# Optimization experiments

Measured on AMD Instinct MI355X. Metric: run time of the kernel, lower is better.

The kernel has to match this reference:

```python
import jax, jax.numpy as jnp
import numpy as np

N_NODES = 100_000
N_EDGES = 1_200_000
IN_C, HID_C, OUT_C, K = 64, 64, 32, 3


def setup_inputs() -> dict:
    key = jax.random.key(0)
    ks = jax.random.split(key, 8)
    x = jax.random.normal(ks[0], (N_NODES, IN_C), dtype=jnp.float32)
    edge_index = jax.random.randint(ks[1], (2, N_EDGES), 0, N_NODES, dtype=jnp.int64)
    # ChebConv parameters: weight [K, in, out], bias [out] (Glorot-ish scale)
    W1 = jax.random.normal(ks[2], (K, IN_C, HID_C), dtype=jnp.float32) / np.sqrt(IN_C)
    b1 = jnp.zeros((HID_C,), dtype=jnp.float32)
    W2 = jax.random.normal(ks[3], (K, HID_C, OUT_C), dtype=jnp.float32) / np.sqrt(HID_C)
    b2 = jnp.zeros((OUT_C,), dtype=jnp.float32)
    return {"x": x, "edge_index": edge_index, "W1": W1, "b1": b1, "W2": W2, "b2": b2}


def _cheb_conv(x, row, col, norm_w, W, b):
    # Scaled Laplacian with lambda_max=2 (PyG default): L_hat = -D^{-1/2} A D^{-1/2}
    def prop(t):  # L_hat @ t, via edge gather + segment-sum scatter
        msg = norm_w[:, None] * t[col]            # [E, C]
        return -jax.ops.segment_sum(msg, row, num_segments=N_NODES)

    Tx0 = x
    out = Tx0 @ W[0]
    Tx1 = prop(x)
    out = out + Tx1 @ W[1]
    for k in range(2, W.shape[0]):
        Tx2 = 2.0 * prop(Tx1) - Tx0          # Chebyshev recurrence
        out = out + Tx2 @ W[k]
        Tx0, Tx1 = Tx1, Tx2
    return out + b


def reference(x, edge_index, W1, b1, W2, b2):
    row, col = edge_index[0], edge_index[1]
    deg = jax.ops.segment_sum(jnp.ones((row.shape[0],), x.dtype), row,
                              num_segments=N_NODES)
    deg_inv_sqrt = jnp.where(deg > 0, jax.lax.rsqrt(jnp.maximum(deg, 1.0)), 0.0)
    norm_w = deg_inv_sqrt[row] * deg_inv_sqrt[col]   # symmetric normalization

    h = jax.nn.relu(_cheb_conv(x, row, col, norm_w, W1, b1))
    # dropout omitted (eval mode / training=False)
    return _cheb_conv(h, row, col, norm_w, W2, b2)
```

## Files before the change

### kernel.cpp

```cpp
#include <hip/hip_runtime.h>
#include <hip/hip_fp16.h>

#define N_NODES_C 100000
#define N_EDGES_C 1200000
#define NBUK ((N_NODES_C + 255) >> 8)
#define CHUNK 4096

typedef _Float16 f16x8 __attribute__((ext_vector_type(8)));
typedef float f32x4 __attribute__((ext_vector_type(4)));

__global__ __launch_bounds__(256) void hist_f2h(const int* __restrict__ ei,
                                                int* __restrict__ bucket_cnt,
                                                const float* __restrict__ x,
                                                __half* __restrict__ xh,
                                                int nedges, int n4, int histB) {
    __shared__ int cnt[NBUK];
    const int tid = threadIdx.x;
    if (blockIdx.x < histB) {
        const int base = blockIdx.x * CHUNK;
        const int nloc = min(CHUNK, nedges - base);
        for (int i = tid; i < NBUK; i += 256) cnt[i] = 0;
        __syncthreads();
        for (int i = tid; i < nloc; i += 256) atomicAdd(&cnt[ei[base + i] >> 8], 1);
        __syncthreads();
        for (int b = tid; b < NBUK; b += 256) {
            int n = cnt[b];
            if (n) atomicAdd(&bucket_cnt[b], n);
        }
    } else {
        int i = (blockIdx.x - histB) * 256 + tid;
        if (i < n4) {
            float4 v = ((const float4*)x)[i];
            __half2 tmp[2];
            tmp[0] = __floats2half2_rn(v.x, v.y);
            tmp[1] = __floats2half2_rn(v.z, v.w);
            ((float2*)xh)[i] = *(float2*)tmp;
        }
    }
}

__global__ __launch_bounds__(256) void bucket_scan(const int* __restrict__ bucket_cnt,
                                                   int* __restrict__ bucket_base,
                                                   int* __restrict__ bucket_next, int nb) {
    __shared__ int s[256];
    const int tid = threadIdx.x;
    int a0 = (2 * tid < nb) ? bucket_cnt[2 * tid] : 0;
    int a1 = (2 * tid + 1 < nb) ? bucket_cnt[2 * tid + 1] : 0;
    s[tid] = a0 + a1;
    __syncthreads();
    for (int off = 1; off < 256; off <<= 1) {
        int v = s[tid];
        int add = (tid >= off) ? s[tid - off] : 0;
        __syncthreads();
        s[tid] = v + add;
        __syncthreads();
    }
    int excl = (tid > 0) ? s[tid - 1] : 0;
    if (2 * tid < nb) { bucket_base[2 * tid] = excl; bucket_next[2 * tid] = excl; }
    if (2 * tid + 1 < nb) { bucket_base[2 * tid + 1] = excl + a0; bucket_next[2 * tid + 1] = excl + a0; }
    if (tid == 255) bucket_base[nb] = s[255];
}

__global__ __launch_bounds__(256) void bin_stage(const int* __restrict__ ei,
                                                 int* __restrict__ bucket_next,
                                                 int2* __restrict__ staged, int nedges) {
    __shared__ int cnt[NBUK];
    __shared__ int ofs[NBUK];
    __shared__ int run[NBUK];
    __shared__ int gbase[NBUK];
    __shared__ int ssum[256];
    __shared__ int2 sedge[CHUNK];
    const int tid = threadIdx.x;
    const int base = blockIdx.x * CHUNK;
    const int nloc = min(CHUNK, nedges - base);

    for (int i = tid; i < NBUK; i += 256) { cnt[i] = 0; run[i] = 0; }
    __syncthreads();

    int r[16], c[16];
#pragma unroll
    for (int k = 0; k < 16; ++k) {
        int loc = tid + k * 256;
        bool ok = loc < nloc;
        int idx = base + loc;
        r[k] = ok ? ei[idx] : -1;
        c[k] = ok ? ei[nedges + idx] : 0;
        if (ok) atomicAdd(&cnt[r[k] >> 8], 1);
    }
    __syncthreads();

    int a0 = (2 * tid < NBUK) ? cnt[2 * tid] : 0;
    int a1 = (2 * tid + 1 < NBUK) ? cnt[2 * tid + 1] : 0;
    ssum[tid] = a0 + a1;
    __syncthreads();
    for (int off = 1; off < 256; off <<= 1) {
        int v = ssum[tid];
        int add = (tid >= off) ? ssum[tid - off] : 0;
        __syncthreads();
        ssum[tid] = v + add;
        __syncthreads();
    }
    int excl = (tid > 0) ? ssum[tid - 1] : 0;
    if (2 * tid < NBUK) ofs[2 * tid] = excl;
    if (2 * tid + 1 < NBUK) ofs[2 * tid + 1] = excl + a0;
    __syncthreads();

#pragma unroll
    for (int k = 0; k < 16; ++k) {
        if (r[k] >= 0) {
            int b = r[k] >> 8;
            int p = atomicAdd(&run[b], 1);
            sedge[ofs[b] + p] = make_int2(r[k], c[k]);
        }
    }
    __syncthreads();

    for (int b = tid; b < NBUK; b += 256) {
        int n = cnt[b];
        gbase[b] = n ? atomicAdd(&bucket_next[b], n) : 0;
    }
    __syncthreads();

    for (int i = tid; i < nloc; i += 256) {
        int2 e = sedge[i];
        int b = e.x >> 8;
        staged[gbase[b] + (i - ofs[b])] = e;
    }
}

__global__ __launch_bounds__(256) void bin_count(const int2* __restrict__ staged,
                                                 const int* __restrict__ bucket_base,
                                                 int* __restrict__ rowptr, float* __restrict__ dis,
                                                 int nnodes, int nedges) {
    __shared__ int deg[256];
    __shared__ int ssum[256];
    const int b = blockIdx.x;
    const int n0 = b << 8;
    const int nend = min(n0 + 256, nnodes);
    const int nloc = nend - n0;
    const int tid = threadIdx.x;
    deg[tid] = 0;
    __syncthreads();
    const int ebase = bucket_base[b];
    const int ecount = bucket_base[b + 1] - ebase;
    for (int i = tid; i < ecount; i += 256) {
        atomicAdd(&deg[staged[ebase + i].x - n0], 1);
    }
    __syncthreads();
    int d = deg[tid];
    if (tid < nloc) {
        float df = (float)d;
        dis[n0 + tid] = (d > 0) ? (1.0f / sqrtf(fmaxf(df, 1.f))) : 0.f;
    }
    ssum[tid] = d;
    __syncthreads();
    for (int off = 1; off < 256; off <<= 1) {
        int v = ssum[tid];
        int add = (tid >= off) ? ssum[tid - off] : 0;
        __syncthreads();
        ssum[tid] = v + add;
        __syncthreads();
    }
    int excl = (tid > 0) ? ssum[tid - 1] : 0;
    if (tid < nloc) rowptr[n0 + tid] = ebase + excl;
    if (b == NBUK - 1 && tid == 0) rowptr[nnodes] = nedges;
}

__global__ __launch_bounds__(256) void bin_place(const int2* __restrict__ staged,
                                                 const int* __restrict__ rowptr,
                                                 const float* __restrict__ dis,
                                                 int2* __restrict__ colw, int nnodes) {
    __shared__ int rp[256];
    __shared__ int nx[256];
    __shared__ float dl[256];
    const int b = blockIdx.x;
    const int n0 = b << 8;
    const int nend = min(n0 + 256, nnodes);
    const int nloc = nend - n0;
    const int tid = threadIdx.x;
    if (tid < nloc) {
        rp[tid] = rowptr[n0 + tid];
        dl[tid] = dis[n0 + tid];
    }
    nx[tid] = 0;
    __syncthreads();
    const int ebase = rowptr[n0];
    const int ecount = rowptr[nend] - ebase;
    for (int i = tid; i < ecount; i += 256) {
        int2 e = staged[ebase + i];
        int rrel = e.x - n0;
        int p = atomicAdd(&nx[rrel], 1);
        float w = -dl[rrel] * dis[e.y];
        colw[rp[rrel] + p] = make_int2(e.y, __float_as_int(w));
    }
}

__global__ void fold_wf(const float* __restrict__ W1, const float* __restrict__ W2,
                        __half* __restrict__ W1f, __half* __restrict__ W2f) {
    int i = blockIdx.x * blockDim.x + threadIdx.x;
    if (i < 12288) {
        int j = i & 7;
        int lane = (i >> 3) & 63;
        int rest = i >> 9;
        int kh = rest % 6;
        int ct = rest / 6;
        int term = kh >> 1;
        int k = ((kh & 1) << 5) | ((lane >> 4) << 3) | j;
        int c = (ct << 4) | (lane & 15);
        float w0 = W1[k * 64 + c];
        float w1 = W1[4096 + k * 64 + c];
        float w2 = W1[2 * 4096 + k * 64 + c];
        float v = (term == 0) ? (w0 - w2) : ((term == 1) ? w1 : 2.0f * w2);
        W1f[i] = __float2half(v);
    } else if (i < 12288 + 6144) {
        int ii = i - 12288;
        int j = ii & 7;
        int lane = (ii >> 3) & 63;
        int rest = ii >> 9;
        int kh = rest & 1;
        int ct = rest >> 1;
        int k = (kh << 5) | ((lane >> 4) << 3) | j;
        int cg = ct * 16 + (lane & 15);
        int seg = cg >> 5;
        int c = cg & 31;
        float w0 = W2[k * 32 + c];
        float w1 = W2[2048 + k * 32 + c];
        float w2 = W2[2 * 2048 + k * 32 + c];
        float v = (seg == 0) ? (w0 - w2) : ((seg == 1) ? w1 : 2.0f * w2);
        W2f[ii] = __float2half(v);
    }
}

__global__ __launch_bounds__(256) void prop_gather_h(const __half* __restrict__ t,
                                                     const int* __restrict__ rowptr,
                                                     const int2* __restrict__ colw,
                                                     __half* __restrict__ out, int nnodes) {
    int node = blockIdx.x * 4 + (threadIdx.x >> 6);
    if (node >= nnodes) return;
    int lane = threadIdx.x & 63;
    int g = lane >> 4;
    int cq = lane & 15;
    int s = rowptr[node];
    int e = rowptr[node + 1];
    float acc[4] = {0.f, 0.f, 0.f, 0.f};
    for (int base = s; base < e; base += 64) {
        int m = e - base;
        if (m > 64) m = 64;
        int2 cw = (lane < m) ? colw[base + lane] : make_int2(0, 0);
        int iters = (m + 3) >> 2;
        int it = 0;
        for (; it + 1 < iters; it += 2) {
            int j0 = (it << 2) | g;
            int j1 = j0 + 4;
            int c0 = __shfl(cw.x, j0);
            float w0 = __int_as_float(__shfl(cw.y, j0));
            int c1 = __shfl(cw.x, j1);
            float w1 = __int_as_float(__shfl(cw.y, j1));
            float2 raw0 = ((const float2*)(t + (size_t)c0 * 64))[cq];
            float2 raw1 = ((const float2*)(t + (size_t)c1 * 64))[cq];
            const __half2* h0 = (const __half2*)&raw0;
            const __half2* h1 = (const __half2*)&raw1;
            float2 f00 = __half22float2(h0[0]);
            float2 f01 = __half22float2(h0[1]);
            float2 f10 = __half22float2(h1[0]);
            float2 f11 = __half22float2(h1[1]);
            acc[0] += w0 * f00.x + w1 * f10.x;
            acc[1] += w0 * f00.y + w1 * f10.y;
            acc[2] += w0 * f01.x + w1 * f11.x;
            acc[3] += w0 * f01.y + w1 * f11.y;
        }
        if (it < iters) {
            int j0 = (it << 2) | g;
            int c0 = __shfl(cw.x, j0);
            float w0 = __int_as_float(__shfl(cw.y, j0));
            float2 raw0 = ((const float2*)(t + (size_t)c0 * 64))[cq];
            const __half2* h0 = (const __half2*)&raw0;
            float2 f00 = __half22float2(h0[0]);
            float2 f01 = __half22float2(h0[1]);
            acc[0] += w0 * f00.x;
            acc[1] += w0 * f00.y;
            acc[2] += w0 * f01.x;
            acc[3] += w0 * f01.y;
        }
    }
#pragma unroll
    for (int i = 0; i < 4; ++i) {
        acc[i] += __shfl_xor(acc[i], 16);
        acc[i] += __shfl_xor(acc[i], 32);
    }
    if (g == 0) {
        __half2 tmp[2];
        tmp[0] = __floats2half2_rn(acc[0], acc[1]);
        tmp[1] = __floats2half2_rn(acc[2], acc[3]);
        ((float2*)(out + (size_t)node * 64))[cq] = *(float2*)tmp;
    }
}

template <bool F32OUT>
__global__ __launch_bounds__(256) void prop_gather32(const __half* __restrict__ t,
                                                     const int* __restrict__ rowptr,
                                                     const int2* __restrict__ colw,
                                                     const void* __restrict__ addin,
                                                     void* __restrict__ outv, int nnodes) {
    int node = blockIdx.x * 4 + (threadIdx.x >> 6);
    if (node >= nnodes) return;
    int lane = threadIdx.x & 63;
    int g = lane >> 4;
    int cq = lane & 15;
    int s = rowptr[node];
    int e = rowptr[node + 1];
    float acc0 = 0.f, acc1 = 0.f;
    for (int base = s; base < e; base += 64) {
        int m = e - base;
        if (m > 64) m = 64;
        int2 cw = (lane < m) ? colw[base + lane] : make_int2(0, 0);
        int iters = (m + 3) >> 2;
        int it = 0;
        for (; it + 1 < iters; it += 2) {
            int j0 = (it << 2) | g;
            int j1 = j0 + 4;
            int c0 = __shfl(cw.x, j0);
            float w0 = __int_as_float(__shfl(cw.y, j0));
            int c1 = __shfl(cw.x, j1);
            float w1 = __int_as_float(__shfl(cw.y, j1));
            __half2 r0 = ((const __half2*)(t + (size_t)c0 * 32))[cq];
            __half2 r1 = ((const __half2*)(t + (size_t)c1 * 32))[cq];
            float2 f0 = __half22float2(r0);
            float2 f1 = __half22float2(r1);
            acc0 += w0 * f0.x + w1 * f1.x;
            acc1 += w0 * f0.y + w1 * f1.y;
        }
        if (it < iters) {
            int j0 = (it << 2) | g;
            int c0 = __shfl(cw.x, j0);
            float w0 = __int_as_float(__shfl(cw.y, j0));
            __half2 r0 = ((const __half2*)(t + (size_t)c0 * 32))[cq];
            float2 f0 = __half22float2(r0);
            acc0 += w0 * f0.x;
            acc1 += w0 * f0.y;
        }
    }
    acc0 += __shfl_xor(acc0, 16); acc1 += __shfl_xor(acc1, 16);
    acc0 += __shfl_xor(acc0, 32); acc1 += __shfl_xor(acc1, 32);
    if (g == 0) {
        if (F32OUT) {
            const float* add = (const float*)addin;
            float* out = (float*)outv;
            float2 a = ((const float2*)(add + (size_t)node * 32))[cq];
            a.x += acc0;
            a.y += acc1;
            ((float2*)(out + (size_t)node * 32))[cq] = a;
        } else {
            const __half* add = (const __half*)addin;
            __half* out = (__half*)outv;
            float2 af = __half22float2(((const __half2*)(add + (size_t)node * 32))[cq]);
            ((__half2*)(out + (size_t)node * 32))[cq] = __floats2half2_rn(acc0 + af.x, acc1 + af.y);
        }
    }
}

__global__ __launch_bounds__(256) void gemm_fused(const __half* __restrict__ A0,
                                                  const __half* __restrict__ A1,
                                                  const __half* __restrict__ A2,
                                                  const __half* __restrict__ W1f,
                                                  const float* __restrict__ b1,
                                                  const __half* __restrict__ W2f,
                                                  const float* __restrict__ b2,
                                                  float* __restrict__ P0,
                                                  __half* __restrict__ G1,
                                                  __half* __restrict__ G2, int nnodes) {
    __shared__ __align__(16) __half htile[4][16 * 72];
    const int wave = threadIdx.x >> 6;
    const int lane = threadIdx.x & 63;
    const int node0 = blockIdx.x * 64 + wave * 16;
    const int m = lane & 15;
    const int quad = lane >> 4;
    int arow = node0 + m;
    if (arow >= nnodes) arow = nnodes - 1;

    const __half* Ap[3] = {A0, A1, A2};
    f16x8 a[6];
#pragma unroll
    for (int kh = 0; kh < 6; ++kh) {
        const __half* A = Ap[kh >> 1];
        a[kh] = *(const f16x8*)(A + (size_t)arow * 64 + ((kh & 1) << 5) + (quad << 3));
    }
    __half* ht = htile[wave];
#pragma unroll
    for (int ct = 0; ct < 4; ++ct) {
        f32x4 acc = {0.f, 0.f, 0.f, 0.f};
#pragma unroll
        for (int kh = 0; kh < 6; ++kh) {
            f16x8 b = *(const f16x8*)(W1f + ((size_t)(ct * 6 + kh) * 64 + lane) * 8);
            acc = __builtin_amdgcn_mfma_f32_16x16x32_f16(a[kh], b, acc, 0, 0, 0);
        }
        int col = (ct << 4) | m;
        float bias = b1[col];
#pragma unroll
        for (int r = 0; r < 4; ++r) {
            ht[(quad * 4 + r) * 72 + col] = __float2half(fmaxf(acc[r] + bias, 0.f));
        }
    }
    __syncthreads();

    f16x8 h0 = *(const f16x8*)(ht + m * 72 + (quad << 3));
    f16x8 h1 = *(const f16x8*)(ht + m * 72 + 32 + (quad << 3));
#pragma unroll
    for (int ct = 0; ct < 6; ++ct) {
        f32x4 acc = {0.f, 0.f, 0.f, 0.f};
        f16x8 b0 = *(const f16x8*)(W2f + ((size_t)(ct * 2 + 0) * 64 + lane) * 8);
        f16x8 b1v = *(const f16x8*)(W2f + ((size_t)(ct * 2 + 1) * 64 + lane) * 8);
        acc = __builtin_amdgcn_mfma_f32_16x16x32_f16(h0, b0, acc, 0, 0, 0);
        acc = __builtin_amdgcn_mfma_f32_16x16x32_f16(h1, b1v, acc, 0, 0, 0);
        int seg = ct >> 1;
        int c = ((ct & 1) << 4) | m;
#pragma unroll
        for (int r = 0; r < 4; ++r) {
            int n = node0 + (quad << 2) + r;
            if (n >= nnodes) continue;
            float v = acc[r];
            if (seg == 0)      P0[(size_t)n * 32 + c] = v + b2[c];
            else if (seg == 1) G1[(size_t)n * 32 + c] = __float2half(v);
            else               G2[(size_t)n * 32 + c] = __float2half(v);
        }
    }
}

extern "C" void kernel_launch(void* const* d_in, const int* in_sizes, int n_in,
                              void* d_out, int out_size, void* d_ws, size_t ws_size,
                              hipStream_t stream) {
    const float* x  = (const float*)d_in[0];
    const int*   ei = (const int*)d_in[1];
    const float* W1 = (const float*)d_in[2];
    const float* b1 = (const float*)d_in[3];
    const float* W2 = (const float*)d_in[4];
    const float* b2 = (const float*)d_in[5];
    float* out = (float*)d_out;

    const int NN = N_NODES_C;
    const int NE = N_EDGES_C;
    const size_t HFEAT_BYTES = (size_t)NN * 64 * sizeof(__half);
    const size_t H32_BYTES = (size_t)NN * 32 * sizeof(__half);

    char* ws = (char*)d_ws;
    size_t off = 0;
    auto alloc = [&](size_t bytes) -> void* {
        void* p = ws + off;
        off += (bytes + 255) & ~(size_t)255;
        return p;
    };
    int*    bucket_cnt  = (int*)alloc((size_t)NBUK * 4);
    int*    bucket_base = (int*)alloc((size_t)(NBUK + 1) * 4);
    int*    bucket_next = (int*)alloc((size_t)NBUK * 4);
    int*    rowptr      = (int*)alloc((size_t)(NN + 1) * 4);
    float*  dis         = (float*)alloc((size_t)NN * 4);
    int2*   staged      = (int2*)alloc((size_t)NE * 8);
    int2*   colw        = (int2*)alloc((size_t)NE * 8);
    __half* xh          = (__half*)alloc(HFEAT_BYTES);
    __half* T1h         = (__half*)alloc(HFEAT_BYTES);
    __half* T2h         = (__half*)alloc(HFEAT_BYTES);
    __half* Qh          = (__half*)alloc(H32_BYTES);
    float*  P0          = (float*)alloc((size_t)NN * 32 * 4);
    __half* W1f         = (__half*)alloc((size_t)4 * 6 * 64 * 8 * 2);
    __half* W2f         = (__half*)alloc((size_t)6 * 2 * 64 * 8 * 2);

    const int PROPB = (NN + 3) / 4;
    const int CONV4 = NN * 64 / 4;
    const int CONVB = (CONV4 + 255) / 256;
    const int BINB = (NE + CHUNK - 1) / CHUNK;
    const int GEMMB = (NN + 63) / 64;

    hipMemsetAsync(bucket_cnt, 0, (size_t)NBUK * 4, stream);
    hist_f2h<<<BINB + CONVB, 256, 0, stream>>>(ei, bucket_cnt, x, xh, NE, CONV4, BINB);
    bucket_scan<<<1, 256, 0, stream>>>(bucket_cnt, bucket_base, bucket_next, NBUK);
    bin_stage<<<BINB, 256, 0, stream>>>(ei, bucket_next, staged, NE);
    bin_count<<<NBUK, 256, 0, stream>>>(staged, bucket_base, rowptr, dis, NN, NE);
    bin_place<<<NBUK, 256, 0, stream>>>(staged, rowptr, dis, colw, NN);
    fold_wf<<<(18432 + 255) / 256, 256, 0, stream>>>(W1, W2, W1f, W2f);

    prop_gather_h<<<PROPB, 256, 0, stream>>>(xh, rowptr, colw, T1h, NN);
    prop_gather_h<<<PROPB, 256, 0, stream>>>(T1h, rowptr, colw, T2h, NN);
    gemm_fused<<<GEMMB, 256, 0, stream>>>(xh, T1h, T2h, W1f, b1, W2f, b2, P0, T1h, T2h, NN);

    prop_gather32<false><<<PROPB, 256, 0, stream>>>(T2h, rowptr, colw, T1h, Qh, NN);
    prop_gather32<true><<<PROPB, 256, 0, stream>>>(Qh, rowptr, colw, P0, out, NN);
}
```

Baseline: 285.3 us.

## Map one node per 8-lane group in CSR gather propagation kernels

Both gather kernels now assign 8 threads per node (32 nodes per block) instead of a full 64-lane wave per node. Each lane loads a wider vector slice of a neighbor row and walks the edge list serially, which removes the shuffle broadcast of column/weight pairs and the cross-lane reduction. With about 12 neighbors per node on average, the old mapping left many lanes idle, and the new one aims to use lanes better and raise memory-level parallelism. In exchange, edge-list loads are repeated across the 8 lanes, and lanes sharing a wave can diverge when node degrees differ.

```diff
diff --git a/kernel.cpp b/kernel.cpp
--- a/kernel.cpp
+++ b/kernel.cpp
@@ -235,65 +235,49 @@
                                                      const int* __restrict__ rowptr,
                                                      const int2* __restrict__ colw,
                                                      __half* __restrict__ out, int nnodes) {
-    int node = blockIdx.x * 4 + (threadIdx.x >> 6);
+    int grp = threadIdx.x >> 3;
+    int ln = threadIdx.x & 7;
+    int node = blockIdx.x * 32 + grp;
     if (node >= nnodes) return;
-    int lane = threadIdx.x & 63;
-    int g = lane >> 4;
-    int cq = lane & 15;
     int s = rowptr[node];
     int e = rowptr[node + 1];
-    float acc[4] = {0.f, 0.f, 0.f, 0.f};
-    for (int base = s; base < e; base += 64) {
-        int m = e - base;
-        if (m > 64) m = 64;
-        int2 cw = (lane < m) ? colw[base + lane] : make_int2(0, 0);
-        int iters = (m + 3) >> 2;
-        int it = 0;
-        for (; it + 1 < iters; it += 2) {
-            int j0 = (it << 2) | g;
-            int j1 = j0 + 4;
-            int c0 = __shfl(cw.x, j0);
-            float w0 = __int_as_float(__shfl(cw.y, j0));
-            int c1 = __shfl(cw.x, j1);
-            float w1 = __int_as_float(__shfl(cw.y, j1));
-            float2 raw0 = ((const float2*)(t + (size_t)c0 * 64))[cq];
-            float2 raw1 = ((const float2*)(t + (size_t)c1 * 64))[cq];
-            const __half2* h0 = (const __half2*)&raw0;
-            const __half2* h1 = (const __half2*)&raw1;
-            float2 f00 = __half22float2(h0[0]);
-            float2 f01 = __half22float2(h0[1]);
-            float2 f10 = __half22float2(h1[0]);
-            float2 f11 = __half22float2(h1[1]);
-            acc[0] += w0 * f00.x + w1 * f10.x;
-            acc[1] += w0 * f00.y + w1 * f10.y;
-            acc[2] += w0 * f01.x + w1 * f11.x;
-            acc[3] += w0 * f01.y + w1 * f11.y;
-        }
-        if (it < iters) {
-            int j0 = (it << 2) | g;
-            int c0 = __shfl(cw.x, j0);
-            float w0 = __int_as_float(__shfl(cw.y, j0));
-            float2 raw0 = ((const float2*)(t + (size_t)c0 * 64))[cq];
-            const __half2* h0 = (const __half2*)&raw0;
-            float2 f00 = __half22float2(h0[0]);
-            float2 f01 = __half22float2(h0[1]);
-            acc[0] += w0 * f00.x;
-            acc[1] += w0 * f00.y;
-            acc[2] += w0 * f01.x;
-            acc[3] += w0 * f01.y;
-        }
-    }
-#pragma unroll
-    for (int i = 0; i < 4; ++i) {
-        acc[i] += __shfl_xor(acc[i], 16);
-        acc[i] += __shfl_xor(acc[i], 32);
-    }
-    if (g == 0) {
-        __half2 tmp[2];
-        tmp[0] = __floats2half2_rn(acc[0], acc[1]);
-        tmp[1] = __floats2half2_rn(acc[2], acc[3]);
-        ((float2*)(out + (size_t)node * 64))[cq] = *(float2*)tmp;
-    }
+    float acc[8] = {0.f, 0.f, 0.f, 0.f, 0.f, 0.f, 0.f, 0.f};
+    int i = s;
+    for (; i + 1 < e; i += 2) {
+        int2 cw0 = colw[i];
+        int2 cw1 = colw[i + 1];
+        float w0 = __int_as_float(cw0.y);
+        float w1 = __int_as_float(cw1.y);
+        float4 r0 = ((const float4*)(t + (size_t)cw0.x * 64))[ln];
+        float4 r1 = ((const float4*)(t + (size_t)cw1.x * 64))[ln];
+        const __half2* h0 = (const __half2*)&r0;
+        const __half2* h1 = (const __half2*)&r1;
+#pragma unroll
+        for (int q = 0; q < 4; ++q) {
+            float2 f0 = __half22float2(h0[q]);
+            float2 f1 = __half22float2(h1[q]);
+            acc[2 * q + 0] += w0 * f0.x + w1 * f1.x;
+            acc[2 * q + 1] += w0 * f0.y + w1 * f1.y;
+        }
+    }
+    if (i < e) {
+        int2 cw0 = colw[i];
+        float w0 = __int_as_float(cw0.y);
+        float4 r0 = ((const float4*)(t + (size_t)cw0.x * 64))[ln];
+        const __half2* h0 = (const __half2*)&r0;
+#pragma unroll
+        for (int q = 0; q < 4; ++q) {
+            float2 f0 = __half22float2(h0[q]);
+            acc[2 * q + 0] += w0 * f0.x;
+            acc[2 * q + 1] += w0 * f0.y;
+        }
+    }
+    __half2 tmp[4];
+    tmp[0] = __floats2half2_rn(acc[0], acc[1]);
+    tmp[1] = __floats2half2_rn(acc[2], acc[3]);
+    tmp[2] = __floats2half2_rn(acc[4], acc[5]);
+    tmp[3] = __floats2half2_rn(acc[6], acc[7]);
+    ((float4*)(out + (size_t)node * 64))[ln] = *(float4*)tmp;
 }
 
 template <bool F32OUT>
@@ -302,60 +286,60 @@
                                                      const int2* __restrict__ colw,
                                                      const void* __restrict__ addin,
                                                      void* __restrict__ outv, int nnodes) {
-    int node = blockIdx.x * 4 + (threadIdx.x >> 6);
+    int grp = threadIdx.x >> 3;
+    int ln = threadIdx.x & 7;
+    int node = blockIdx.x * 32 + grp;
     if (node >= nnodes) return;
-    int lane = threadIdx.x & 63;
-    int g = lane >> 4;
-    int cq = lane & 15;
     int s = rowptr[node];
     int e = rowptr[node + 1];
-    float acc0 = 0.f, acc1 = 0.f;
-    for (int base = s; base < e; base += 64) {
-        int m = e - base;
-        if (m > 64) m = 64;
-        int2 cw = (lane < m) ? colw[base + lane] : make_int2(0, 0);
-        int iters = (m + 3) >> 2;
-        int it = 0;
-        for (; it + 1 < iters; it += 2) {
-            int j0 = (it << 2) | g;
-            int j1 = j0 + 4;
-            int c0 = __shfl(cw.x, j0);
-            float w0 = __int_as_float(__shfl(cw.y, j0));
-            int c1 = __shfl(cw.x, j1);
-            float w1 = __int_as_float(__shfl(cw.y, j1));
-            __half2 r0 = ((const __half2*)(t + (size_t)c0 * 32))[cq];
-            __half2 r1 = ((const __half2*)(t + (size_t)c1 * 32))[cq];
-            float2 f0 = __half22float2(r0);
-            float2 f1 = __half22float2(r1);
-            acc0 += w0 * f0.x + w1 * f1.x;
-            acc1 += w0 * f0.y + w1 * f1.y;
-        }
-        if (it < iters) {
-            int j0 = (it << 2) | g;
-            int c0 = __shfl(cw.x, j0);
-            float w0 = __int_as_float(__shfl(cw.y, j0));
-            __half2 r0 = ((const __half2*)(t + (size_t)c0 * 32))[cq];
-            float2 f0 = __half22float2(r0);
-            acc0 += w0 * f0.x;
-            acc1 += w0 * f0.y;
-        }
-    }
-    acc0 += __shfl_xor(acc0, 16); acc1 += __shfl_xor(acc1, 16);
-    acc0 += __shfl_xor(acc0, 32); acc1 += __shfl_xor(acc1, 32);
-    if (g == 0) {
-        if (F32OUT) {
-            const float* add = (const float*)addin;
-            float* out = (float*)outv;
-            float2 a = ((const float2*)(add + (size_t)node * 32))[cq];
-            a.x += acc0;
-            a.y += acc1;
-            ((float2*)(out + (size_t)node * 32))[cq] = a;
-        } else {
-            const __half* add = (const __half*)addin;
-            __half* out = (__half*)outv;
-            float2 af = __half22float2(((const __half2*)(add + (size_t)node * 32))[cq]);
-            ((__half2*)(out + (size_t)node * 32))[cq] = __floats2half2_rn(acc0 + af.x, acc1 + af.y);
-        }
+    float acc[4] = {0.f, 0.f, 0.f, 0.f};
+    int i = s;
+    for (; i + 1 < e; i += 2) {
+        int2 cw0 = colw[i];
+        int2 cw1 = colw[i + 1];
+        float w0 = __int_as_float(cw0.y);
+        float w1 = __int_as_float(cw1.y);
+        float2 r0 = ((const float2*)(t + (size_t)cw0.x * 32))[ln];
+        float2 r1 = ((const float2*)(t + (size_t)cw1.x * 32))[ln];
+        const __half2* h0 = (const __half2*)&r0;
+        const __half2* h1 = (const __half2*)&r1;
+#pragma unroll
+        for (int q = 0; q < 2; ++q) {
+            float2 f0 = __half22float2(h0[q]);
+            float2 f1 = __half22float2(h1[q]);
+            acc[2 * q + 0] += w0 * f0.x + w1 * f1.x;
+            acc[2 * q + 1] += w0 * f0.y + w1 * f1.y;
+        }
+    }
+    if (i < e) {
+        int2 cw0 = colw[i];
+        float w0 = __int_as_float(cw0.y);
+        float2 r0 = ((const float2*)(t + (size_t)cw0.x * 32))[ln];
+        const __half2* h0 = (const __half2*)&r0;
+#pragma unroll
+        for (int q = 0; q < 2; ++q) {
+            float2 f0 = __half22float2(h0[q]);
+            acc[2 * q + 0] += w0 * f0.x;
+            acc[2 * q + 1] += w0 * f0.y;
+        }
+    }
+    if (F32OUT) {
+        const float* add = (const float*)addin;
+        float* out = (float*)outv;
+        float4 a = ((const float4*)(add + (size_t)node * 32))[ln];
+        a.x += acc[0]; a.y += acc[1]; a.z += acc[2]; a.w += acc[3];
+        ((float4*)(out + (size_t)node * 32))[ln] = a;
+    } else {
+        const __half* add = (const __half*)addin;
+        __half* out = (__half*)outv;
+        float2 raw = ((const float2*)(add + (size_t)node * 32))[ln];
+        const __half2* hp = (const __half2*)&raw;
+        float2 a0 = __half22float2(hp[0]);
+        float2 a1 = __half22float2(hp[1]);
+        __half2 tmp[2];
+        tmp[0] = __floats2half2_rn(acc[0] + a0.x, acc[1] + a0.y);
+        tmp[1] = __floats2half2_rn(acc[2] + a1.x, acc[3] + a1.y);
+        ((float2*)(out + (size_t)node * 32))[ln] = *(float2*)tmp;
     }
 }
 
@@ -464,7 +448,7 @@
     __half* W1f         = (__half*)alloc((size_t)4 * 6 * 64 * 8 * 2);
     __half* W2f         = (__half*)alloc((size_t)6 * 2 * 64 * 8 * 2);
 
-    const int PROPB = (NN + 3) / 4;
+    const int PROPB = (NN + 31) / 32;
     const int CONV4 = NN * 64 / 4;
     const int CONVB = (CONV4 + 255) / 256;
     const int BINB = (NE + CHUNK - 1) / CHUNK;
```

Result: faster. 256.1 us (-10.2%).
